# Performance work log

Hardware: AMD Instinct MI355X
Metric: run time of the kernel (lower is better)

The kernel has to match this reference:

```python
import jax, jax.numpy as jnp
import numpy as np


def setup_inputs() -> dict:
    key = jax.random.key(0)
    k1, k2, k3 = jax.random.split(key, 3)
    B, C, Z, S, T, H = 8, 128, 4, 8, 1024, 64
    WQ = jax.random.normal(k1, (C, Z, S, H), dtype=jnp.float32)
    WK = jax.random.normal(k2, (B, Z, T, H), dtype=jnp.float32)
    K = jax.random.normal(k3, (B, Z, T, H), dtype=jnp.float32)
    return {"WQ": WQ, "WK": WK, "K": K}


def reference(WQ, WK, K):
    # tanh non-linearities on keys (WQ is used raw, as in the original)
    WKt = jnp.tanh(WK)          # [b,z,t,h]
    Kt = jnp.tanh(K)            # [b,z,t,h]
    # attention scores per (batch, code, group, synonym) over tokens t
    scores = jnp.einsum('bzth,czsh->bczst', WKt, WQ)   # [b,c,z,s,t]
    attn = jax.nn.softmax(scores, axis=-1)             # softmax over t
    # weighted sum of (tanh'd) values over tokens
    context = jnp.einsum('bzth,bczst->bczsh', Kt, attn)  # [b,c,z,s,h]
    # AvgPool3d((1, s, 1)) then squeeze(-2) == mean over synonym axis s
    context = jnp.mean(context, axis=3)                  # [b,c,z,h]
    return (scores, context, attn)
```

## Files before the change

### kernel.cpp

```cpp
#include <hip/hip_runtime.h>

typedef _Float16 f16;
typedef f16 f16x4 __attribute__((ext_vector_type(4)));
typedef f16 f16x8 __attribute__((ext_vector_type(8)));
typedef float f32x16 __attribute__((ext_vector_type(16)));

#define NB 8
#define NC 128
#define NZ 4
#define NS 8
#define NT 1024
#define NH 64

#define WQ_N (NC*NZ*NS*NH)
#define WK_N (NB*NZ*NT*NH)

#define OUT_CTX  (NB*NC*NZ*NS*NT)
#define OUT_ATTN (OUT_CTX + NB*NC*NZ*NH)

__device__ __forceinline__ float fast_tanh(float x) {
    float e = __expf(2.0f * x);
    return 1.0f - 2.0f * __builtin_amdgcn_rcpf(e + 1.0f);
}

__global__ __launch_bounds__(256) void prep_kernel(
    const float* __restrict__ WQ, const float* __restrict__ WK, const float* __restrict__ K,
    f16* __restrict__ wqh, f16* __restrict__ wkh, f16* __restrict__ ktT)
{
    __shared__ f16 ldsT[64*64];
    const int tid = threadIdx.x;
    const int blk = blockIdx.x;
    if (blk < 512) {
        const int bz = blk >> 4;
        const int t0 = (blk & 15) << 6;
        #pragma unroll
        for (int it = 0; it < 4; ++it) {
            int idx = it*256 + tid;
            int tl  = idx >> 4;
            int seg = idx & 15;
            int gi  = (bz*NT + t0 + tl)*NH + seg*4;
            float4 wk4 = *(const float4*)(WK + gi);
            float4 k4  = *(const float4*)(K  + gi);
            f16x4 wv;
            wv[0] = (f16)fast_tanh(wk4.x);
            wv[1] = (f16)fast_tanh(wk4.y);
            wv[2] = (f16)fast_tanh(wk4.z);
            wv[3] = (f16)fast_tanh(wk4.w);
            *(f16x4*)(wkh + gi) = wv;
            ldsT[(seg*4+0)*64 + tl] = (f16)fast_tanh(k4.x);
            ldsT[(seg*4+1)*64 + tl] = (f16)fast_tanh(k4.y);
            ldsT[(seg*4+2)*64 + tl] = (f16)fast_tanh(k4.z);
            ldsT[(seg*4+3)*64 + tl] = (f16)fast_tanh(k4.w);
        }
        __syncthreads();
        #pragma unroll
        for (int it = 0; it < 4; ++it) {
            int idx = it*256 + tid;
            int h  = idx >> 4;
            int ts = idx & 15;
            f16x4 v = *(const f16x4*)&ldsT[h*64 + ts*4];
            *(f16x4*)(ktT + (bz*NH + h)*NT + t0 + ts*4) = v;
        }
    } else {
        const int ib = blk - 512;
        #pragma unroll
        for (int it = 0; it < 16; ++it) {
            int gi = ib*16384 + it*1024 + tid*4;
            float4 q = *(const float4*)(WQ + gi);
            f16x4 w;
            w[0] = (f16)q.x; w[1] = (f16)q.y; w[2] = (f16)q.z; w[3] = (f16)q.w;
            *(f16x4*)(wqh + gi) = w;
        }
    }
}

__global__ __launch_bounds__(256, 2) void fused_kernel(
    const f16* __restrict__ wqh, const f16* __restrict__ wkh, const f16* __restrict__ ktT,
    float* __restrict__ scores, float* __restrict__ attn, float* __restrict__ ctxout)
{
    __shared__ float rsL[4][32];
    __shared__ float invL[32];
    __shared__ f16   attnB[4][1024];
    __shared__ float ctxW[4][32][64];

    const int tid  = threadIdx.x;
    const int wave = tid >> 6;
    const int lane = tid & 63;
    const int l31  = lane & 31;
    const int g    = lane >> 5;
    const int bid  = blockIdx.x;
    const int bz = bid & 31, mt = bid >> 5;
    const int b = bz >> 2, z = bz & 3;
    const int m0 = mt * 32;

    const int mgA = m0 + l31;
    const f16* ap = wqh + (((mgA >> 3)*NZ + z)*NS + (mgA & 7))*NH + g*8;
    f16x8 afr[4];
    #pragma unroll
    for (int st = 0; st < 4; ++st) afr[st] = *(const f16x8*)(ap + st*16);

    f32x16 acc[8];
    #pragma unroll
    for (int tt = 0; tt < 8; ++tt)
        #pragma unroll
        for (int r = 0; r < 16; ++r) acc[tt][r] = 0.f;

    #pragma unroll
    for (int tt = 0; tt < 8; ++tt) {
        const int t0 = (tt*4 + wave) * 32;
        const f16* bp = wkh + (bz*NT + t0 + l31)*NH + g*8;
        #pragma unroll
        for (int st = 0; st < 4; ++st) {
            f16x8 bfr = *(const f16x8*)(bp + st*16);
            acc[tt] = __builtin_amdgcn_mfma_f32_32x32x16_f16(afr[st], bfr, acc[tt], 0, 0, 0);
        }
    }

    const int base2 = ((b*NC + mt*4)*NZ + z)*NS*NT;
    float p[16];
    #pragma unroll
    for (int r = 0; r < 16; ++r) p[r] = 0.f;

    #pragma unroll
    for (int tt = 0; tt < 8; ++tt) {
        const int tcol = (tt*4 + wave)*32 + l31;
        #pragma unroll
        for (int r = 0; r < 16; ++r) {
            int off = base2 + (r >> 2)*32768 + ((r & 3) + 4*g)*1024 + tcol;
            float v = acc[tt][r];
            scores[off] = v;
            float e = __expf(v);
            acc[tt][r] = e;
            p[r] += e;
        }
    }

    #pragma unroll
    for (int d = 1; d < 32; d <<= 1)
        #pragma unroll
        for (int r = 0; r < 16; ++r) p[r] += __shfl_xor(p[r], d, 64);

    if (l31 == 0) {
        #pragma unroll
        for (int r = 0; r < 16; ++r) rsL[wave][(r & 3) + 8*(r >> 2) + 4*g] = p[r];
    }
    __syncthreads();
    if (tid < 32) invL[tid] = 1.0f / (rsL[0][tid] + rsL[1][tid] + rsL[2][tid] + rsL[3][tid]);
    __syncthreads();

    f32x16 cacc[2];
    #pragma unroll
    for (int nt = 0; nt < 2; ++nt)
        #pragma unroll
        for (int r = 0; r < 16; ++r) cacc[nt][r] = 0.f;

    #pragma unroll
    for (int tt = 0; tt < 8; ++tt) {
        const int t0 = (tt*4 + wave) * 32;
        const int tcol = t0 + l31;
        #pragma unroll
        for (int r = 0; r < 16; ++r) {
            int ml = (r & 3) + 8*(r >> 2) + 4*g;
            float a = acc[tt][r] * invL[ml];
            int off = base2 + (r >> 2)*32768 + ((r & 3) + 4*g)*1024 + tcol;
            attn[off] = a;
            int tb = l31 >> 3;
            int ai = ((tb*32 + ml)*8 + (l31 & 7)) ^ (tb << 3);
            attnB[wave][ai] = (f16)a;
        }
        #pragma unroll
        for (int s2 = 0; s2 < 2; ++s2) {
            int tb = 2*s2 + g;
            int ai = ((tb*32 + l31)*8) ^ (tb << 3);
            f16x8 pa = *(const f16x8*)&attnB[wave][ai];
            #pragma unroll
            for (int nt = 0; nt < 2; ++nt) {
                const f16* bp2 = ktT + (bz*NH + nt*32 + l31)*NT + t0 + s2*16 + g*8;
                f16x8 bf = *(const f16x8*)bp2;
                cacc[nt] = __builtin_amdgcn_mfma_f32_32x32x16_f16(pa, bf, cacc[nt], 0, 0, 0);
            }
        }
    }

    #pragma unroll
    for (int nt = 0; nt < 2; ++nt) {
        #pragma unroll
        for (int r = 0; r < 16; ++r) {
            int ml = (r & 3) + 8*(r >> 2) + 4*g;
            ctxW[wave][ml][nt*32 + l31] = cacc[nt][r];
        }
    }
    __syncthreads();

    {
        int cl = tid >> 6;
        int h  = tid & 63;
        float sum = 0.f;
        #pragma unroll
        for (int w = 0; w < 4; ++w)
            #pragma unroll
            for (int q = 0; q < 8; ++q)
                sum += ctxW[w][cl*8 + q][h];
        ctxout[((b*NC + (m0 >> 3) + cl)*NZ + z)*NH + h] = sum * 0.125f;
    }
}

extern "C" void kernel_launch(void* const* d_in, const int* in_sizes, int n_in,
                              void* d_out, int out_size, void* d_ws, size_t ws_size,
                              hipStream_t stream)
{
    const float* WQ = (const float*)d_in[0];
    const float* WK = (const float*)d_in[1];
    const float* K  = (const float*)d_in[2];

    char* ws = (char*)d_ws;
    f16* wqh = (f16*)(ws);
    f16* wkh = (f16*)(ws + (size_t)WQ_N*2);
    f16* ktT = (f16*)(ws + (size_t)WQ_N*2 + (size_t)WK_N*2);

    float* out    = (float*)d_out;
    float* scores = out;
    float* ctxout = out + OUT_CTX;
    float* attn   = out + OUT_ATTN;

    hipLaunchKernelGGL(prep_kernel, dim3(528), dim3(256), 0, stream,
                       WQ, WK, K, wqh, wkh, ktT);
    hipLaunchKernelGGL(fused_kernel, dim3(1024), dim3(256), 0, stream,
                       wqh, wkh, ktT, scores, attn, ctxout);
}
```

Before: 71.07 us.

## Transpose score MFMA, vectorize score/attn stores, replace LDS staging with permlane swap

Swaps the MFMA operand order so each lane holds scores for one query row across consecutive tokens. This lets scores and attn be written as float4 vectors instead of scattered scalar stores. It also reduces the row-sum reduction to a single cross-half shuffle, and the separate invL barrier goes away. The LDS attnB staging used to build the second MFMA's A operand is replaced by packed fp16 conversion plus v_permlane32_swap, and conversion now uses round-toward-zero, which could slightly change precision.

```diff
diff --git a/kernel.cpp b/kernel.cpp
--- a/kernel.cpp
+++ b/kernel.cpp
@@ -4,6 +4,8 @@
 typedef f16 f16x4 __attribute__((ext_vector_type(4)));
 typedef f16 f16x8 __attribute__((ext_vector_type(8)));
 typedef float f32x16 __attribute__((ext_vector_type(16)));
+typedef unsigned int u32;
+typedef u32 u32x4 __attribute__((ext_vector_type(4)));
 
 #define NB 8
 #define NC 128
@@ -79,8 +81,6 @@
     float* __restrict__ scores, float* __restrict__ attn, float* __restrict__ ctxout)
 {
     __shared__ float rsL[4][32];
-    __shared__ float invL[32];
-    __shared__ f16   attnB[4][1024];
     __shared__ float ctxW[4][32][64];
 
     const int tid  = threadIdx.x;
@@ -93,60 +93,48 @@
     const int b = bz >> 2, z = bz & 3;
     const int m0 = mt * 32;
 
-    const int mgA = m0 + l31;
-    const f16* ap = wqh + (((mgA >> 3)*NZ + z)*NS + (mgA & 7))*NH + g*8;
-    f16x8 afr[4];
-    #pragma unroll
-    for (int st = 0; st < 4; ++st) afr[st] = *(const f16x8*)(ap + st*16);
+    const int m = m0 + l31;
+    const f16* ap = wqh + (((m >> 3)*NZ + z)*NS + (m & 7))*NH + g*8;
+    f16x8 qfr[4];
+    #pragma unroll
+    for (int st = 0; st < 4; ++st) qfr[st] = *(const f16x8*)(ap + st*16);
+
+    const int rowbase = (((b*NC + (m >> 3))*NZ + z)*NS + (m & 7))*NT;
 
     f32x16 acc[8];
-    #pragma unroll
-    for (int tt = 0; tt < 8; ++tt)
-        #pragma unroll
-        for (int r = 0; r < 16; ++r) acc[tt][r] = 0.f;
+    float p = 0.f;
 
     #pragma unroll
     for (int tt = 0; tt < 8; ++tt) {
         const int t0 = (tt*4 + wave) * 32;
-        const f16* bp = wkh + (bz*NT + t0 + l31)*NH + g*8;
+        const f16* kp = wkh + (bz*NT + t0 + l31)*NH + g*8;
+        #pragma unroll
+        for (int r = 0; r < 16; ++r) acc[tt][r] = 0.f;
         #pragma unroll
         for (int st = 0; st < 4; ++st) {
-            f16x8 bfr = *(const f16x8*)(bp + st*16);
-            acc[tt] = __builtin_amdgcn_mfma_f32_32x32x16_f16(afr[st], bfr, acc[tt], 0, 0, 0);
-        }
-    }
-
-    const int base2 = ((b*NC + mt*4)*NZ + z)*NS*NT;
-    float p[16];
-    #pragma unroll
-    for (int r = 0; r < 16; ++r) p[r] = 0.f;
-
-    #pragma unroll
-    for (int tt = 0; tt < 8; ++tt) {
-        const int tcol = (tt*4 + wave)*32 + l31;
+            f16x8 kfr = *(const f16x8*)(kp + st*16);
+            acc[tt] = __builtin_amdgcn_mfma_f32_32x32x16_f16(kfr, qfr[st], acc[tt], 0, 0, 0);
+        }
+        float* sp = scores + rowbase + t0 + 4*g;
+        #pragma unroll
+        for (int q = 0; q < 4; ++q) {
+            float4 v;
+            v.x = acc[tt][4*q+0]; v.y = acc[tt][4*q+1];
+            v.z = acc[tt][4*q+2]; v.w = acc[tt][4*q+3];
+            *(float4*)(sp + 8*q) = v;
+        }
         #pragma unroll
         for (int r = 0; r < 16; ++r) {
-            int off = base2 + (r >> 2)*32768 + ((r & 3) + 4*g)*1024 + tcol;
-            float v = acc[tt][r];
-            scores[off] = v;
-            float e = __expf(v);
+            float e = __expf(acc[tt][r]);
             acc[tt][r] = e;
-            p[r] += e;
-        }
-    }
-
-    #pragma unroll
-    for (int d = 1; d < 32; d <<= 1)
-        #pragma unroll
-        for (int r = 0; r < 16; ++r) p[r] += __shfl_xor(p[r], d, 64);
-
-    if (l31 == 0) {
-        #pragma unroll
-        for (int r = 0; r < 16; ++r) rsL[wave][(r & 3) + 8*(r >> 2) + 4*g] = p[r];
-    }
+            p += e;
+        }
+    }
+
+    p += __shfl_xor(p, 32);
+    if (lane < 32) rsL[wave][l31] = p;
     __syncthreads();
-    if (tid < 32) invL[tid] = 1.0f / (rsL[0][tid] + rsL[1][tid] + rsL[2][tid] + rsL[3][tid]);
-    __syncthreads();
+    const float inv = 1.0f / (rsL[0][l31] + rsL[1][l31] + rsL[2][l31] + rsL[3][l31]);
 
     f32x16 cacc[2];
     #pragma unroll
@@ -157,27 +145,35 @@
     #pragma unroll
     for (int tt = 0; tt < 8; ++tt) {
         const int t0 = (tt*4 + wave) * 32;
-        const int tcol = t0 + l31;
-        #pragma unroll
-        for (int r = 0; r < 16; ++r) {
-            int ml = (r & 3) + 8*(r >> 2) + 4*g;
-            float a = acc[tt][r] * invL[ml];
-            int off = base2 + (r >> 2)*32768 + ((r & 3) + 4*g)*1024 + tcol;
-            attn[off] = a;
-            int tb = l31 >> 3;
-            int ai = ((tb*32 + ml)*8 + (l31 & 7)) ^ (tb << 3);
-            attnB[wave][ai] = (f16)a;
-        }
-        #pragma unroll
-        for (int s2 = 0; s2 < 2; ++s2) {
-            int tb = 2*s2 + g;
-            int ai = ((tb*32 + l31)*8) ^ (tb << 3);
-            f16x8 pa = *(const f16x8*)&attnB[wave][ai];
+        #pragma unroll
+        for (int r = 0; r < 16; ++r) acc[tt][r] *= inv;
+        float* apn = attn + rowbase + t0 + 4*g;
+        #pragma unroll
+        for (int q = 0; q < 4; ++q) {
+            float4 v;
+            v.x = acc[tt][4*q+0]; v.y = acc[tt][4*q+1];
+            v.z = acc[tt][4*q+2]; v.w = acc[tt][4*q+3];
+            *(float4*)(apn + 8*q) = v;
+        }
+        u32 pkA[4], pkB[4];
+        #pragma unroll
+        for (int q = 0; q < 4; ++q) {
+            pkA[q] = __builtin_bit_cast(u32, __builtin_amdgcn_cvt_pkrtz(acc[tt][4*q+0], acc[tt][4*q+1]));
+            pkB[q] = __builtin_bit_cast(u32, __builtin_amdgcn_cvt_pkrtz(acc[tt][4*q+2], acc[tt][4*q+3]));
+        }
+        #pragma unroll
+        for (int q2 = 0; q2 < 2; ++q2) {
+            u32 u0 = pkA[2*q2], u2 = pkA[2*q2 + 1];
+            u32 u1 = pkB[2*q2], u3 = pkB[2*q2 + 1];
+            asm volatile("v_permlane32_swap_b32 %0, %1" : "+v"(u0), "+v"(u2));
+            asm volatile("v_permlane32_swap_b32 %0, %1" : "+v"(u1), "+v"(u3));
+            u32x4 uv; uv[0] = u0; uv[1] = u1; uv[2] = u2; uv[3] = u3;
+            f16x8 af = __builtin_bit_cast(f16x8, uv);
             #pragma unroll
             for (int nt = 0; nt < 2; ++nt) {
-                const f16* bp2 = ktT + (bz*NH + nt*32 + l31)*NT + t0 + s2*16 + g*8;
+                const f16* bp2 = ktT + (bz*NH + nt*32 + l31)*NT + t0 + q2*16 + g*8;
                 f16x8 bf = *(const f16x8*)bp2;
-                cacc[nt] = __builtin_amdgcn_mfma_f32_32x32x16_f16(pa, bf, cacc[nt], 0, 0, 0);
+                cacc[nt] = __builtin_amdgcn_mfma_f32_32x32x16_f16(af, bf, cacc[nt], 0, 0, 0);
             }
         }
     }
```

New measurement: 85.24 us. 1.2x slower.
